# Kernel optimization log

Measured on AMD Instinct MI355X. Metric: run time of the kernel, lower is better.

## Reference

```python
import jax, jax.numpy as jnp
import numpy as np

COST_CLASS = 1.0
COST_L1 = 1.0


def _lsa(cost):
    """Exact rectangular linear sum assignment (Jonker-Volgenant / e-maxx Hungarian).
    cost: (n, m) numpy float64 with n <= m. Returns ans[n]: column assigned to each row.
    """
    n, m = cost.shape
    INF = np.inf
    u = np.zeros(n + 1)
    v = np.zeros(m + 1)
    p = np.zeros(m + 1, dtype=np.int64)    # p[j]: 1-indexed row matched to column j (0 = free)
    way = np.zeros(m + 1, dtype=np.int64)
    for i in range(1, n + 1):
        p[0] = i
        j0 = 0
        minv = np.full(m + 1, INF)
        used = np.zeros(m + 1, dtype=bool)
        while True:
            used[j0] = True
            i0 = p[j0]
            minv1 = minv[1:]               # view, in-place updates propagate
            jmask = ~used[1:]
            cur = cost[i0 - 1, :] - u[i0] - v[1:]
            upd = jmask & (cur < minv1)
            minv1[upd] = cur[upd]
            way[1:][upd] = j0
            idx = np.nonzero(jmask)[0]
            j1rel = idx[np.argmin(minv1[idx])]
            delta = minv1[j1rel]
            u[p[used]] += delta
            v[used] -= delta
            minv1[jmask] -= delta
            j0 = j1rel + 1
            if p[j0] == 0:
                break
        # augment along the alternating path
        while j0:
            j1 = way[j0]
            p[j0] = p[j1]
            j0 = j1
    ans = np.zeros(n, dtype=np.int64)
    for j in range(1, m + 1):
        if p[j] > 0:
            ans[p[j] - 1] = j - 1
    return ans


def _solve_blocks(blocks):
    """blocks: (B, Q, T) numpy. Per-batch optimal assignment, scipy-compatible output:
    row_ind sorted ascending, min(Q,T) pairs (here Q >= T so T pairs)."""
    blocks = np.asarray(blocks, dtype=np.float64)
    B, Q, T = blocks.shape
    rows = np.empty((B, T), dtype=np.int32)
    cols = np.empty((B, T), dtype=np.int32)
    for b in range(B):
        c = blocks[b]
        if Q >= T:
            ans = _lsa(c.T)                      # ans[t] = matched query q
            order = np.argsort(ans, kind="stable")
            rows[b] = ans[order]
            cols[b] = order
        else:
            ans = _lsa(c)
            rows[b] = np.arange(Q)
            cols[b] = ans
    return rows, cols


def _cost_blocks(outputs, targets):
    """Diagonal (per-sample) blocks of the DETR cost matrix.
    outputs: (B, Q, 1+P); targets: (B, T, 1+P). Returns (B, Q, T).
    Math identical to building the full (B*Q, B*T) matrix and slicing, as in the source."""
    out_prob = jax.nn.softmax(outputs[:, :, 0], axis=-1)      # softmax over the QUERY axis (as in source)
    out_pos = outputs[:, :, 1:]                                # (B, Q, P)
    tgt_pos = targets[:, :, 1:]                                # (B, T, P)
    cost_l1 = jnp.abs(out_pos[:, :, None, :] - tgt_pos[:, None, :, :]).sum(-1)  # L1 cdist, (B, Q, T)
    return COST_CLASS * (-out_prob[:, :, None]) + COST_L1 * cost_l1


def setup_inputs() -> dict:
    key = jax.random.key(0)
    k1, k2 = jax.random.split(key)
    outputs = jax.random.normal(k1, (8, 2048, 3), dtype=jnp.float32)
    targets = jax.random.uniform(k2, (8, 256, 3), dtype=jnp.float32)
    return {"outputs": outputs, "targets": targets}


def reference(outputs, targets):
    blocks = _cost_blocks(outputs, targets)                    # (B, Q, T)
    B, Q, T = blocks.shape
    n = min(Q, T)
    shapes = (jax.ShapeDtypeStruct((B, n), jnp.int32),
              jax.ShapeDtypeStruct((B, n), jnp.int32))
    row_ind, col_ind = jax.pure_callback(_solve_blocks, shapes, blocks)
    return row_ind, col_ind
```

## Files before the change

kernel.cpp:

```cpp
#include <hip/hip_runtime.h>


constexpr int B = 8;
constexpr int Q = 2048;
constexpr int T = 256;
constexpr int NT = 256;
constexpr int KPT = Q / NT;
constexpr int NW = NT / 64;
constexpr double DINF = 1e300;

struct __align__(16) CD { double u; float tx, ty; };

__device__ __forceinline__ unsigned wave_min_u32_dpp(unsigned a) {
  int v = (int)a, t;
  t = __builtin_amdgcn_update_dpp(v, v, 0x111, 0xf, 0xf, false);
  v = ((unsigned)t < (unsigned)v) ? t : v;
  t = __builtin_amdgcn_update_dpp(v, v, 0x112, 0xf, 0xf, false);
  v = ((unsigned)t < (unsigned)v) ? t : v;
  t = __builtin_amdgcn_update_dpp(v, v, 0x114, 0xf, 0xf, false);
  v = ((unsigned)t < (unsigned)v) ? t : v;
  t = __builtin_amdgcn_update_dpp(v, v, 0x118, 0xf, 0xf, false);
  v = ((unsigned)t < (unsigned)v) ? t : v;
  t = __builtin_amdgcn_update_dpp(v, v, 0x142, 0xf, 0xf, false);
  v = ((unsigned)t < (unsigned)v) ? t : v;
  t = __builtin_amdgcn_update_dpp(v, v, 0x143, 0xf, 0xf, false);
  v = ((unsigned)t < (unsigned)v) ? t : v;
  return (unsigned)__builtin_amdgcn_readlane(v, 63);
}

__launch_bounds__(NT, 1)
__global__ void hungarian_r9(const float* __restrict__ outs,
                             const float* __restrict__ tgts,
                             int* __restrict__ out) {
  const int b = blockIdx.x;
  const int tid = threadIdx.x;
  const int lane = tid & 63;
  const int wv = tid >> 6;

  __shared__ CD colDat[Q + 1];
  __shared__ CD rowDat[T + 1];
  __shared__ short p[Q + 1];
  __shared__ short visCol[T + 8];
  __shared__ double visD[T + 8];
  __shared__ uint4 pk[2][NW];
  __shared__ int ansArr[T];
  __shared__ double s_rv[NW];
  __shared__ float sh_f;

  const size_t qbase = (size_t)b * Q;
  const size_t tbase = (size_t)b * T;

  float xs[KPT], qx[KPT], qy[KPT];
#pragma unroll
  for (int k = 0; k < KPT; ++k) {
    const size_t o = (qbase + tid + k * NT) * 3;
    xs[k] = outs[o];
    qx[k] = outs[o + 1];
    qy[k] = outs[o + 2];
  }
  {
    const size_t o = (tbase + tid) * 3;
    rowDat[tid + 1].tx = tgts[o + 1];
    rowDat[tid + 1].ty = tgts[o + 2];
    rowDat[tid + 1].u = 0.0;
    if (tid == 0) { rowDat[0].tx = 0.f; rowDat[0].ty = 0.f; rowDat[0].u = 0.0; }
  }

  float lmax = xs[0];
#pragma unroll
  for (int k = 1; k < KPT; ++k) lmax = fmaxf(lmax, xs[k]);
  for (int off = 32; off > 0; off >>= 1) lmax = fmaxf(lmax, __shfl_down(lmax, off));
  if ((tid & 63) == 0) s_rv[tid >> 6] = (double)lmax;
  __syncthreads();
  if (tid == 0) {
    float m2 = (float)s_rv[0];
    for (int w = 1; w < NW; ++w) m2 = fmaxf(m2, (float)s_rv[w]);
    sh_f = m2;
  }
  __syncthreads();
  const float smax = sh_f;
  float ex[KPT];
  float lsum = 0.f;
#pragma unroll
  for (int k = 0; k < KPT; ++k) { ex[k] = expf(xs[k] - smax); lsum += ex[k]; }
  for (int off = 32; off > 0; off >>= 1) lsum += __shfl_down(lsum, off);
  if ((tid & 63) == 0) s_rv[tid >> 6] = (double)lsum;
  __syncthreads();
  if (tid == 0) {
    float s2 = 0.f;
    for (int w = 0; w < NW; ++w) s2 += (float)s_rv[w];
    sh_f = s2;
  }
  __syncthreads();
  const float ssum = sh_f;
  float np_[KPT];
#pragma unroll
  for (int k = 0; k < KPT; ++k) np_[k] = -(ex[k] / ssum);

  for (int j = tid; j <= Q; j += NT) {
    p[j] = 0;
    CD c0; c0.u = 0.0; c0.tx = -1.0f; c0.ty = 0.0f;
    colDat[j] = c0;
  }
  double vreg[KPT];
#pragma unroll
  for (int k = 0; k < KPT; ++k) vreg[k] = 0.0;
  __syncthreads();

  for (int i = 1; i <= T; ++i) {
    unsigned usedMask = 0;
    double D = 0.0;
    int i0 = i;
    double ui0 = rowDat[i].u;
    float tX = rowDat[i].tx, tY = rowDat[i].ty;
    int s = 0, S;
    int recRow = 0, recCol = 0;
    double recU = 0.0, recD = 0.0;
    float recTX = 0.f, recTY = 0.f;

    for (;;) {
      if (tid == s) { recRow = i0; recU = ui0; recTX = tX; recTY = tY; recD = D; }

      double cv[KPT];
#pragma unroll
      for (int k = 0; k < KPT; ++k) {
        const float cf = fabsf(qx[k] - tX) + fabsf(qy[k] - tY) + np_[k];
        double cur = ((double)cf - ui0) - vreg[k];
        if (usedMask & (1u << k)) cur = DINF;
        cv[k] = cur;
      }
      const double m01 = fmin(cv[0], cv[1]), m23 = fmin(cv[2], cv[3]);
      const double m45 = fmin(cv[4], cv[5]), m67 = fmin(cv[6], cv[7]);
      const double m03 = fmin(m01, m23), m47 = fmin(m45, m67);
      double bval = fmin(m03, m47);
      unsigned emsk = 0;
#pragma unroll
      for (int k = 0; k < KPT; ++k) emsk |= (cv[k] == bval) ? (1u << k) : 0u;
      const int bk = (int)__builtin_ctz(emsk);
      int bidx = 1 + tid + (bk << 8);

      bval += 0.0;
      const long long bb = __double_as_longlong(bval);
      const unsigned long long key = (unsigned long long)bb ^
          ((bb < 0) ? 0xFFFFFFFFFFFFFFFFull : 0x8000000000000000ull);
      const unsigned khi = (unsigned)(key >> 32);
      const unsigned klo = (unsigned)key;

      const unsigned minhi = wave_min_u32_dpp(khi);
      const unsigned long long mask = __ballot(khi == minhi);
      unsigned wklo; int widx;
      if (__popcll(mask) == 1) {
        const int wl = (int)__ffsll(mask) - 1;
        wklo = (unsigned)__builtin_amdgcn_readlane((int)klo, wl);
        widx = __builtin_amdgcn_readlane(bidx, wl);
      } else {
        wklo = 0xffffffffu; widx = 0x7fffffff;
        unsigned long long mm = mask;
        while (mm) {
          const int l = (int)__ffsll(mm) - 1; mm &= mm - 1;
          const unsigned lo2 = (unsigned)__builtin_amdgcn_readlane((int)klo, l);
          const int ix2 = __builtin_amdgcn_readlane(bidx, l);
          if (lo2 < wklo || (lo2 == wklo && ix2 < widx)) { wklo = lo2; widx = ix2; }
        }
      }
      const int par = s & 1;
      if (lane == 0) pk[par][wv] = make_uint4(minhi, wklo, (unsigned)widx, 0u);
      __syncthreads();

      const uint4 c0v = pk[par][0];
      const uint4 c1v = pk[par][1];
      const uint4 c2v = pk[par][2];
      const uint4 c3v = pk[par][3];
      const CD cd0 = colDat[(int)c0v.z];
      const CD cd1 = colDat[(int)c1v.z];
      const CD cd2 = colDat[(int)c2v.z];
      const CD cd3 = colDat[(int)c3v.z];

      const unsigned long long k0b = ((unsigned long long)c0v.x << 32) | c0v.y;
      const unsigned long long k1b = ((unsigned long long)c1v.x << 32) | c1v.y;
      const unsigned long long k2b = ((unsigned long long)c2v.x << 32) | c2v.y;
      const unsigned long long k3b = ((unsigned long long)c3v.x << 32) | c3v.y;
      const int j0b = (int)c0v.z, j1bb = (int)c1v.z;
      const int j2b = (int)c2v.z, j3b = (int)c3v.z;
      const bool w01 = (k1b < k0b) || (k1b == k0b && j1bb < j0b);
      const unsigned long long k01 = w01 ? k1b : k0b;
      const int j01 = w01 ? j1bb : j0b;
      const bool w23 = (k3b < k2b) || (k3b == k2b && j3b < j2b);
      const unsigned long long k23 = w23 ? k3b : k2b;
      const int j23 = w23 ? j3b : j2b;
      const bool wf = (k23 < k01) || (k23 == k01 && j23 < j01);
      const unsigned long long bkk = wf ? k23 : k01;
      const int j1 = wf ? j23 : j01;
      CD cdA; cdA.u = w01 ? cd1.u : cd0.u;
      cdA.tx = w01 ? cd1.tx : cd0.tx; cdA.ty = w01 ? cd1.ty : cd0.ty;
      CD cdB; cdB.u = w23 ? cd3.u : cd2.u;
      cdB.tx = w23 ? cd3.tx : cd2.tx; cdB.ty = w23 ? cd3.ty : cd2.ty;
      CD cd; cd.u = wf ? cdB.u : cdA.u;
      cd.tx = wf ? cdB.tx : cdA.tx; cd.ty = wf ? cdB.ty : cdA.ty;

      const long long db = (long long)((bkk & 0x8000000000000000ull)
                                           ? (bkk ^ 0x8000000000000000ull) : ~bkk);
      D += __longlong_as_double(db);
      if (tid == ((j1 - 1) & 255)) usedMask |= 1u << ((j1 - 1) >> 8);
      if (tid == s) recCol = j1;
      const int pj1 = (int)p[j1];
      ++s;
      if (cd.tx < 0.0f) { S = s; break; }
      ui0 = cd.u; tX = cd.tx; tY = cd.ty; i0 = pj1;
    }

    __syncthreads();
    const double Dfin = D;
    if (tid < S) {
      visCol[tid + 1] = (short)recCol;
      visD[tid] = recD;
      p[recCol] = (short)recRow;
      const double unew = recU + (Dfin - recD);
      rowDat[recRow].u = unew;
      CD c2; c2.u = unew; c2.tx = recTX; c2.ty = recTY;
      colDat[recCol] = c2;
    }
    __syncthreads();
    for (int sv = 1; sv < S; ++sv) {
      const int qv = (int)visCol[sv] - 1;
      if ((qv & 255) == tid) vreg[qv >> 8] -= (Dfin - visD[sv]);
    }
  }
  __syncthreads();

  for (int j = 1 + tid; j <= Q; j += NT) {
    const int pi = (int)p[j];
    if (pi > 0) ansArr[pi - 1] = j - 1;
  }
  __syncthreads();
  const int a = ansArr[tid];
  int rank = 0;
  for (int t2 = 0; t2 < T; ++t2) rank += (ansArr[t2] < a) ? 1 : 0;
  out[(size_t)b * T + rank] = a;
  out[(size_t)B * T + (size_t)b * T + rank] = tid;
}

extern "C" void kernel_launch(void* const* d_in, const int* in_sizes, int n_in,
                              void* d_out, int out_size, void* d_ws, size_t ws_size,
                              hipStream_t stream) {
  const float* outs = (const float*)d_in[0];
  const float* tgts = (const float*)d_in[1];
  int* out = (int*)d_out;
  hungarian_r9<<<B, NT, 0, stream>>>(outs, tgts, out);
}
```

Measured before the change: 910.3 us.

## Keep column state in registers and publish winner data with the reduction

Each thread now keeps the per-column dual and target-coordinate data for the columns it owns in registers. The winning lane of each wave writes that data next to its reduction key, which removes the dependent shared-memory gather of column data after the barrier in the inner Dijkstra step. The serial per-row loop over visited columns that updated column potentials is replaced by a scatter into per-thread slots, followed by a fixed unrolled read of those slots. The cost is more registers, more shared memory and a larger packet per step, and the slot scheme depends on idempotent re-reads of stale entries.

Result: slower. 1.176 ms (+29.1%).

```diff
diff --git a/kernel.cpp b/kernel.cpp
--- a/kernel.cpp
+++ b/kernel.cpp
@@ -29,23 +29,23 @@
 }
 
 __launch_bounds__(NT, 1)
-__global__ void hungarian_r9(const float* __restrict__ outs,
-                             const float* __restrict__ tgts,
-                             int* __restrict__ out) {
+__global__ void hungarian_r10(const float* __restrict__ outs,
+                              const float* __restrict__ tgts,
+                              int* __restrict__ out) {
   const int b = blockIdx.x;
   const int tid = threadIdx.x;
   const int lane = tid & 63;
   const int wv = tid >> 6;
 
-  __shared__ CD colDat[Q + 1];
   __shared__ CD rowDat[T + 1];
   __shared__ short p[Q + 1];
-  __shared__ short visCol[T + 8];
-  __shared__ double visD[T + 8];
-  __shared__ uint4 pk[2][NW];
+  __shared__ uint4 pkA[2][NW];
+  __shared__ uint4 pkB[2][NW];
   __shared__ int ansArr[T];
   __shared__ double s_rv[NW];
   __shared__ float sh_f;
+  __shared__ CD cdSlot[KPT][NT];
+  __shared__ double vdelta[KPT][NT];
 
   const size_t qbase = (size_t)b * Q;
   const size_t tbase = (size_t)b * T;
@@ -97,14 +97,18 @@
 #pragma unroll
   for (int k = 0; k < KPT; ++k) np_[k] = -(ex[k] / ssum);
 
-  for (int j = tid; j <= Q; j += NT) {
-    p[j] = 0;
-    CD c0; c0.u = 0.0; c0.tx = -1.0f; c0.ty = 0.0f;
-    colDat[j] = c0;
-  }
+  for (int j = tid; j <= Q; j += NT) p[j] = 0;
   double vreg[KPT];
-#pragma unroll
-  for (int k = 0; k < KPT; ++k) vreg[k] = 0.0;
+  double cdu[KPT];
+  float cdx[KPT], cdy[KPT];
+#pragma unroll
+  for (int k = 0; k < KPT; ++k) {
+    vreg[k] = 0.0;
+    cdu[k] = 0.0; cdx[k] = -1.0f; cdy[k] = 0.0f;
+    vdelta[k][tid] = 0.0;
+    CD z; z.u = 0.0; z.tx = -2.0f; z.ty = 0.0f;
+    cdSlot[k][tid] = z;
+  }
   __syncthreads();
 
   for (int i = 1; i <= T; ++i) {
@@ -114,12 +118,15 @@
     double ui0 = rowDat[i].u;
     float tX = rowDat[i].tx, tY = rowDat[i].ty;
     int s = 0, S;
-    int recRow = 0, recCol = 0;
+    int j1v = 0;
+    int recRow = 0, recCol = 0, recPrev = 0;
     double recU = 0.0, recD = 0.0;
     float recTX = 0.f, recTY = 0.f;
 
     for (;;) {
-      if (tid == s) { recRow = i0; recU = ui0; recTX = tX; recTY = tY; recD = D; }
+      if (tid == s) {
+        recRow = i0; recU = ui0; recTX = tX; recTY = tY; recD = D; recPrev = j1v;
+      }
 
       double cv[KPT];
 #pragma unroll
@@ -137,7 +144,21 @@
 #pragma unroll
       for (int k = 0; k < KPT; ++k) emsk |= (cv[k] == bval) ? (1u << k) : 0u;
       const int bk = (int)__builtin_ctz(emsk);
-      int bidx = 1 + tid + (bk << 8);
+      const int bidx = 1 + tid + (bk << 8);
+
+      const int b0 = bk & 1, b1 = (bk >> 1) & 1, b2 = (bk >> 2) & 1;
+      const double uA = b0 ? cdu[1] : cdu[0], uB = b0 ? cdu[3] : cdu[2];
+      const double uC = b0 ? cdu[5] : cdu[4], uD = b0 ? cdu[7] : cdu[6];
+      const float xA = b0 ? cdx[1] : cdx[0], xB = b0 ? cdx[3] : cdx[2];
+      const float xC = b0 ? cdx[5] : cdx[4], xD = b0 ? cdx[7] : cdx[6];
+      const float yA = b0 ? cdy[1] : cdy[0], yB = b0 ? cdy[3] : cdy[2];
+      const float yC = b0 ? cdy[5] : cdy[4], yD = b0 ? cdy[7] : cdy[6];
+      const double uE = b1 ? uB : uA, uF = b1 ? uD : uC;
+      const float xE = b1 ? xB : xA, xF = b1 ? xD : xC;
+      const float yE = b1 ? yB : yA, yF = b1 ? yD : yC;
+      const double csu = b2 ? uF : uE;
+      const float csx = b2 ? xF : xE;
+      const float csy = b2 ? yF : yE;
 
       bval += 0.0;
       const long long bb = __double_as_longlong(bval);
@@ -148,33 +169,39 @@
 
       const unsigned minhi = wave_min_u32_dpp(khi);
       const unsigned long long mask = __ballot(khi == minhi);
-      unsigned wklo; int widx;
+      int wl;
       if (__popcll(mask) == 1) {
-        const int wl = (int)__ffsll(mask) - 1;
-        wklo = (unsigned)__builtin_amdgcn_readlane((int)klo, wl);
-        widx = __builtin_amdgcn_readlane(bidx, wl);
+        wl = (int)__ffsll(mask) - 1;
       } else {
-        wklo = 0xffffffffu; widx = 0x7fffffff;
+        unsigned wklo = 0xffffffffu; int widx = 0x7fffffff; wl = 0;
         unsigned long long mm = mask;
         while (mm) {
           const int l = (int)__ffsll(mm) - 1; mm &= mm - 1;
           const unsigned lo2 = (unsigned)__builtin_amdgcn_readlane((int)klo, l);
           const int ix2 = __builtin_amdgcn_readlane(bidx, l);
-          if (lo2 < wklo || (lo2 == wklo && ix2 < widx)) { wklo = lo2; widx = ix2; }
+          if (lo2 < wklo || (lo2 == wklo && ix2 < widx)) {
+            wklo = lo2; widx = ix2; wl = l;
+          }
         }
       }
       const int par = s & 1;
-      if (lane == 0) pk[par][wv] = make_uint4(minhi, wklo, (unsigned)widx, 0u);
+      if (lane == wl) {
+        pkA[par][wv] = make_uint4(minhi, klo, (unsigned)bidx, 0u);
+        const long long cl = __double_as_longlong(csu);
+        pkB[par][wv] = make_uint4((unsigned)(unsigned long long)cl,
+                                  (unsigned)((unsigned long long)cl >> 32),
+                                  __float_as_uint(csx), __float_as_uint(csy));
+      }
       __syncthreads();
 
-      const uint4 c0v = pk[par][0];
-      const uint4 c1v = pk[par][1];
-      const uint4 c2v = pk[par][2];
-      const uint4 c3v = pk[par][3];
-      const CD cd0 = colDat[(int)c0v.z];
-      const CD cd1 = colDat[(int)c1v.z];
-      const CD cd2 = colDat[(int)c2v.z];
-      const CD cd3 = colDat[(int)c3v.z];
+      const uint4 c0v = pkA[par][0];
+      const uint4 c1v = pkA[par][1];
+      const uint4 c2v = pkA[par][2];
+      const uint4 c3v = pkA[par][3];
+      const uint4 d0v = pkB[par][0];
+      const uint4 d1v = pkB[par][1];
+      const uint4 d2v = pkB[par][2];
+      const uint4 d3v = pkB[par][3];
 
       const unsigned long long k0b = ((unsigned long long)c0v.x << 32) | c0v.y;
       const unsigned long long k1b = ((unsigned long long)c1v.x << 32) | c1v.y;
@@ -182,6 +209,18 @@
       const unsigned long long k3b = ((unsigned long long)c3v.x << 32) | c3v.y;
       const int j0b = (int)c0v.z, j1bb = (int)c1v.z;
       const int j2b = (int)c2v.z, j3b = (int)c3v.z;
+      const double u0 = __longlong_as_double(
+          (long long)(((unsigned long long)d0v.y << 32) | d0v.x));
+      const double u1 = __longlong_as_double(
+          (long long)(((unsigned long long)d1v.y << 32) | d1v.x));
+      const double u2 = __longlong_as_double(
+          (long long)(((unsigned long long)d2v.y << 32) | d2v.x));
+      const double u3 = __longlong_as_double(
+          (long long)(((unsigned long long)d3v.y << 32) | d3v.x));
+      const float x0 = __uint_as_float(d0v.z), y0 = __uint_as_float(d0v.w);
+      const float x1 = __uint_as_float(d1v.z), y1 = __uint_as_float(d1v.w);
+      const float x2 = __uint_as_float(d2v.z), y2 = __uint_as_float(d2v.w);
+      const float x3 = __uint_as_float(d3v.z), y3 = __uint_as_float(d3v.w);
       const bool w01 = (k1b < k0b) || (k1b == k0b && j1bb < j0b);
       const unsigned long long k01 = w01 ? k1b : k0b;
       const int j01 = w01 ? j1bb : j0b;
@@ -191,12 +230,12 @@
       const bool wf = (k23 < k01) || (k23 == k01 && j23 < j01);
       const unsigned long long bkk = wf ? k23 : k01;
       const int j1 = wf ? j23 : j01;
-      CD cdA; cdA.u = w01 ? cd1.u : cd0.u;
-      cdA.tx = w01 ? cd1.tx : cd0.tx; cdA.ty = w01 ? cd1.ty : cd0.ty;
-      CD cdB; cdB.u = w23 ? cd3.u : cd2.u;
-      cdB.tx = w23 ? cd3.tx : cd2.tx; cdB.ty = w23 ? cd3.ty : cd2.ty;
-      CD cd; cd.u = wf ? cdB.u : cdA.u;
-      cd.tx = wf ? cdB.tx : cdA.tx; cd.ty = wf ? cdB.ty : cdA.ty;
+      const double uAx = w01 ? u1 : u0, uBx = w23 ? u3 : u2;
+      const float xAx = w01 ? x1 : x0, xBx = w23 ? x3 : x2;
+      const float yAx = w01 ? y1 : y0, yBx = w23 ? y3 : y2;
+      const double cdun = wf ? uBx : uAx;
+      const float cdtx = wf ? xBx : xAx;
+      const float cdty = wf ? yBx : yAx;
 
       const long long db = (long long)((bkk & 0x8000000000000000ull)
                                            ? (bkk ^ 0x8000000000000000ull) : ~bkk);
@@ -204,26 +243,37 @@
       if (tid == ((j1 - 1) & 255)) usedMask |= 1u << ((j1 - 1) >> 8);
       if (tid == s) recCol = j1;
       const int pj1 = (int)p[j1];
+      j1v = j1;
       ++s;
-      if (cd.tx < 0.0f) { S = s; break; }
-      ui0 = cd.u; tX = cd.tx; tY = cd.ty; i0 = pj1;
+      if (cdtx < 0.0f) { S = s; break; }
+      ui0 = cdun; tX = cdtx; tY = cdty; i0 = pj1;
     }
 
     __syncthreads();
     const double Dfin = D;
     if (tid < S) {
-      visCol[tid + 1] = (short)recCol;
-      visD[tid] = recD;
       p[recCol] = (short)recRow;
       const double unew = recU + (Dfin - recD);
       rowDat[recRow].u = unew;
+      const int c = recCol - 1;
       CD c2; c2.u = unew; c2.tx = recTX; c2.ty = recTY;
-      colDat[recCol] = c2;
+      cdSlot[c >> 8][c & 255] = c2;
+      if (tid >= 1) {
+        const int pc = recPrev - 1;
+        vdelta[pc >> 8][pc & 255] = -(Dfin - recD);
+      }
     }
     __syncthreads();
-    for (int sv = 1; sv < S; ++sv) {
-      const int qv = (int)visCol[sv] - 1;
-      if ((qv & 255) == tid) vreg[qv >> 8] -= (Dfin - visD[sv]);
+#pragma unroll
+    for (int k = 0; k < KPT; ++k) {
+      const double dv = vdelta[k][tid];
+      const CD sl = cdSlot[k][tid];
+      vreg[k] += dv;
+      vdelta[k][tid] = 0.0;
+      const bool upd = (sl.tx > -1.5f);
+      cdu[k] = upd ? sl.u : cdu[k];
+      cdx[k] = upd ? sl.tx : cdx[k];
+      cdy[k] = upd ? sl.ty : cdy[k];
     }
   }
   __syncthreads();
@@ -246,5 +296,5 @@
   const float* outs = (const float*)d_in[0];
   const float* tgts = (const float*)d_in[1];
   int* out = (int*)d_out;
-  hungarian_r9<<<B, NT, 0, stream>>>(outs, tgts, out);
+  hungarian_r10<<<B, NT, 0, stream>>>(outs, tgts, out);
 }
```
